# Optimization experiments

Hardware: AMD Instinct MI355X
Metric: run time of the kernel (lower is better)

## Reference

```python
import jax, jax.numpy as jnp
import numpy as np

B = 16384        # batch (population evaluation batch)
NUM_IN = 256     # input nodes
N = 1024         # total nodes
K = 8            # max fan-in (padded)
NN = N - NUM_IN  # non-input nodes, in topo order
NUM_OUT = 64


def setup_inputs() -> dict:
    key = jax.random.key(0)
    k0, k1, k2 = jax.random.split(key, 3)
    inputs = jax.random.normal(k0, (B, NUM_IN), dtype=jnp.float32)

    # Build a random DAG: node i (i >= NUM_IN) draws up to K predecessors from {0..i-1}.
    rng = np.random.default_rng(0)
    in_idx = np.zeros((NN, K), dtype=np.int32)
    edge_mask = np.zeros((NN, K), dtype=bool)
    for r in range(NN):
        node = NUM_IN + r
        deg = min(K, node)
        preds = rng.choice(node, size=deg, replace=False)
        in_idx[r, :deg] = preds
        edge_mask[r, :deg] = True

    edge_w = jax.random.normal(k1, (NN, K), dtype=jnp.float32) * 0.5
    bias = jax.random.normal(k2, (NN,), dtype=jnp.float32) * 0.1
    response = jnp.ones((NN,), dtype=jnp.float32)
    out_idx = jnp.arange(NUM_IN, N, dtype=jnp.int32)          # topo order of non-input nodes
    output_idx = jnp.arange(N - NUM_OUT, N, dtype=jnp.int32)  # output nodes
    return {
        "inputs": inputs, "edge_w": edge_w, "bias": bias, "response": response,
        "in_idx": jnp.asarray(in_idx), "edge_mask": jnp.asarray(edge_mask),
        "out_idx": out_idx, "output_idx": output_idx,
    }


def reference(inputs, edge_w, bias, response, in_idx, edge_mask, out_idx, output_idx):
    b = inputs.shape[0]
    num_in = inputs.shape[1]
    n = num_in + out_idx.shape[0]
    # node_vals[:, input_idx] = inputs  (input_idx == arange(num_in))
    node_vals = jnp.zeros((b, n), dtype=jnp.float32).at[:, :num_in].set(inputs)

    def step(carry, xs):
        idx_r, w_r, m_r, b_r, resp_r, o_r = xs
        # gather incoming node values [B, K], apply per-edge weight (conn gene)
        vals = carry[:, idx_r]
        s = jnp.sum(jnp.where(m_r, vals * w_r, 0.0), axis=1)  # node aggregation: sum
        y = jnp.tanh(b_r + resp_r * s)                        # node gene activation
        carry = carry.at[:, o_r].set(y)
        return carry, None

    node_vals, _ = jax.lax.scan(
        step, node_vals, (in_idx, edge_w, edge_mask, bias, response, out_idx)
    )
    return node_vals[:, output_idx]
```

## Files before the change

kernel.cpp:

```cpp
#include <hip/hip_runtime.h>
#include <stdint.h>
#include <stddef.h>

#define B_TOT   16384
#define NUM_IN  256
#define N_NODES 1024
#define NN      768
#define K       8
#define NUM_OUT 64
#define NB      64
#define MAXL    800
#define TPB     1024
#define WPB     16

typedef _Float16 h2 __attribute__((ext_vector_type(2)));

struct Rec {
  uint32_t p[8];
  uint32_t w01, w23, w45, w67;
  uint32_t outPh;
  float    bias;
  uint32_t pad0, pad1;
};
static_assert(sizeof(Rec) == 64, "Rec must be 64B");

__global__ __launch_bounds__(NN)
void setup_kernel(const int* __restrict__ in_idx,
                  const float* __restrict__ edge_w,
                  const float* __restrict__ bias,
                  const float* __restrict__ response,
                  const int* __restrict__ out_idx,
                  int* __restrict__ g_nlev,
                  int* __restrict__ g_loff,
                  Rec* __restrict__ recs)
{
  __shared__ int lvl[N_NODES];
  __shared__ int hist[MAXL];
  __shared__ int cnt[MAXL];
  __shared__ int offs[MAXL + 2];
  __shared__ int changed;
  __shared__ int maxlv;

  const int t = threadIdx.x;

  for (int i = t; i < N_NODES; i += NN) lvl[i] = 0;
  for (int i = t; i < MAXL; i += NN) { hist[i] = 0; cnt[i] = 0; }
  if (t == 0) maxlv = 0;

  int idxs[K];
#pragma unroll
  for (int k = 0; k < K; ++k)
    idxs[k] = in_idx[t * K + k];
  __syncthreads();

  for (int iter = 0; iter < 800; ++iter) {
    int nl = 0;
#pragma unroll
    for (int k = 0; k < K; ++k) {
      int l = lvl[idxs[k]];
      nl = (l > nl) ? l : nl;
    }
    nl += 1;
    __syncthreads();
    if (t == 0) changed = 0;
    int cur = lvl[NUM_IN + t];
    __syncthreads();
    if (nl != cur) { lvl[NUM_IN + t] = nl; changed = 1; }
    __syncthreads();
    if (changed == 0) break;
  }

  const int L = lvl[NUM_IN + t];
  atomicAdd(&hist[L], 1);
  atomicMax(&maxlv, L);
  __syncthreads();
  const int ml = maxlv;
  if (t == 0) {
    offs[1] = 0;
    for (int l = 1; l <= ml; ++l) offs[l + 1] = offs[l] + hist[l];
  }
  __syncthreads();
  const int pos = offs[L] + atomicAdd(&cnt[L], 1);

  Rec r;
#pragma unroll
  for (int k = 0; k < K; ++k) {
    uint32_t id = (uint32_t)idxs[k];
    r.p[k] = id * 64u + ((id & 31u) << 1);
  }
  const float rsp = response[t];
  uint16_t hw[K];
#pragma unroll
  for (int k = 0; k < K; ++k) {
    _Float16 h = (_Float16)(edge_w[t * K + k] * rsp);
    hw[k] = __builtin_bit_cast(uint16_t, h);
  }
  r.w01 = (uint32_t)hw[0] | ((uint32_t)hw[1] << 16);
  r.w23 = (uint32_t)hw[2] | ((uint32_t)hw[3] << 16);
  r.w45 = (uint32_t)hw[4] | ((uint32_t)hw[5] << 16);
  r.w67 = (uint32_t)hw[6] | ((uint32_t)hw[7] << 16);
  uint32_t oid = (uint32_t)out_idx[t];
  r.outPh = oid * 64u + ((oid & 31u) << 1);
  r.bias = bias[t];
  r.pad0 = 0; r.pad1 = 0;
  recs[pos] = r;

  if (t <= ml) g_loff[t] = offs[t + 1];
  if (t == 0)  g_nlev[0] = ml;
}

__global__ __launch_bounds__(TPB, 4)
void eval_kernel(const float* __restrict__ inputs,
                 const int* __restrict__ output_idx,
                 const int* __restrict__ g_nlev,
                 const int* __restrict__ g_loff,
                 const Rec* __restrict__ recs,
                 float* __restrict__ out)
{
  __shared__ _Float16 vals[N_NODES * NB];
  __shared__ int      loffs[MAXL + 1];

  const uint32_t tid  = threadIdx.x;
  const uint32_t lane = tid & 63u;
  const uint32_t wave = tid >> 6;
  const int      base = blockIdx.x * NB;

  const int nlev = g_nlev[0];
  for (int i = (int)tid; i <= nlev; i += TPB) loffs[i] = g_loff[i];

  const uint32_t col = tid & 255u;
  const uint32_t cg  = tid >> 8;
  const uint32_t swz = col * 64u + ((col & 31u) << 1);
  for (uint32_t c = cg; c < NB; c += 4) {
    float v = inputs[(size_t)(base + c) * NUM_IN + col];
    vals[swz ^ c] = (_Float16)v;
  }
  __syncthreads();

  for (int l = 0; l < nlev; ++l) {
    const int beg = loffs[l], end = loffs[l + 1];
    int j = beg + (int)wave;
    if (j < end) {
      Rec rr = recs[__builtin_amdgcn_readfirstlane(j)];
      for (;;) {
        const int jn = j + WPB;
        const bool has = jn < end;
        Rec rn;
        if (has) rn = recs[__builtin_amdgcn_readfirstlane(jn)];

        const _Float16 x0 = vals[rr.p[0] ^ lane];
        const _Float16 x1 = vals[rr.p[1] ^ lane];
        const _Float16 x2 = vals[rr.p[2] ^ lane];
        const _Float16 x3 = vals[rr.p[3] ^ lane];
        const _Float16 x4 = vals[rr.p[4] ^ lane];
        const _Float16 x5 = vals[rr.p[5] ^ lane];
        const _Float16 x6 = vals[rr.p[6] ^ lane];
        const _Float16 x7 = vals[rr.p[7] ^ lane];

        const h2 v01 = {x0, x1};
        const h2 v23 = {x2, x3};
        const h2 v45 = {x4, x5};
        const h2 v67 = {x6, x7};

#if __has_builtin(__builtin_amdgcn_fdot2)
        float x = rr.bias;
        x = __builtin_amdgcn_fdot2(v01, __builtin_bit_cast(h2, rr.w01), x, false);
        x = __builtin_amdgcn_fdot2(v23, __builtin_bit_cast(h2, rr.w23), x, false);
        x = __builtin_amdgcn_fdot2(v45, __builtin_bit_cast(h2, rr.w45), x, false);
        x = __builtin_amdgcn_fdot2(v67, __builtin_bit_cast(h2, rr.w67), x, false);
#else
        const h2 w01 = __builtin_bit_cast(h2, rr.w01);
        const h2 w23 = __builtin_bit_cast(h2, rr.w23);
        const h2 w45 = __builtin_bit_cast(h2, rr.w45);
        const h2 w67 = __builtin_bit_cast(h2, rr.w67);
        float s0 = __builtin_fmaf((float)w01.x, (float)v01.x, rr.bias);
        float s1 = (float)w01.y * (float)v01.y;
        float s2 = (float)w23.x * (float)v23.x;
        float s3 = (float)w23.y * (float)v23.y;
        s0 = __builtin_fmaf((float)w45.x, (float)v45.x, s0);
        s1 = __builtin_fmaf((float)w45.y, (float)v45.y, s1);
        s2 = __builtin_fmaf((float)w67.x, (float)v67.x, s2);
        s3 = __builtin_fmaf((float)w67.y, (float)v67.y, s3);
        float x = (s0 + s1) + (s2 + s3);
#endif

        const float e  = __expf(x + x);
        const float rc = __builtin_amdgcn_rcpf(e + 1.0f);
        const float y  = __builtin_fmaf(-2.0f, rc, 1.0f);

        vals[rr.outPh ^ lane] = (_Float16)y;

        if (!has) break;
        rr = rn; j = jn;
      }
    }
    __syncthreads();
  }

  const uint32_t oid  = (uint32_t)output_idx[lane];
  const uint32_t oswz = oid * 64u + ((oid & 31u) << 1);
  for (uint32_t k = 0; k < 4; ++k) {
    const uint32_t b = wave + k * 16u;
    float v = (float)vals[oswz ^ b];
    out[(size_t)(base + b) * NUM_OUT + lane] = v;
  }
}

extern "C" void kernel_launch(void* const* d_in, const int* in_sizes, int n_in,
                              void* d_out, int out_size, void* d_ws, size_t ws_size,
                              hipStream_t stream)
{
  (void)in_sizes; (void)n_in; (void)out_size; (void)ws_size;

  const float* inputs     = (const float*)d_in[0];
  const float* edge_w     = (const float*)d_in[1];
  const float* bias       = (const float*)d_in[2];
  const float* response   = (const float*)d_in[3];
  const int*   in_idx     = (const int*)d_in[4];
  const int*   out_idx    = (const int*)d_in[6];
  const int*   output_idx = (const int*)d_in[7];
  float*       out        = (float*)d_out;

  char* ws = (char*)d_ws;
  int* g_nlev = (int*)ws;
  int* g_loff = (int*)(ws + 256);
  Rec* recs   = (Rec*)(ws + 8192);

  hipLaunchKernelGGL(setup_kernel, dim3(1), dim3(NN), 0, stream,
                     in_idx, edge_w, bias, response, out_idx,
                     g_nlev, g_loff, recs);
  hipLaunchKernelGGL(eval_kernel, dim3(B_TOT / NB), dim3(TPB), 0, stream,
                     inputs, output_idx, g_nlev, g_loff, recs, out);
}
```

Before: 128.3 us.

## Software-pipeline LDS gathers across nodes, use byte offsets, double-buffer level setup

The eval loop now issues the next node's eight LDS gathers before computing the current node's dot product and tanh, so LDS latency overlaps with arithmetic. Precomputed offsets are stored as byte offsets to drop a shift per access. The setup kernel's level propagation moves to Jacobi-style double buffering and checks convergence only every fourth iteration, which cuts barriers. The risk is higher register pressure under the 4-waves launch bound. Within a level, loads of the next node are safe because nodes in the same level do not depend on each other.

```diff
diff --git a/kernel.cpp b/kernel.cpp
--- a/kernel.cpp
+++ b/kernel.cpp
@@ -34,7 +34,8 @@
                   int* __restrict__ g_loff,
                   Rec* __restrict__ recs)
 {
-  __shared__ int lvl[N_NODES];
+  __shared__ int lvlA[N_NODES];
+  __shared__ int lvlB[N_NODES];
   __shared__ int hist[MAXL];
   __shared__ int cnt[MAXL];
   __shared__ int offs[MAXL + 2];
@@ -43,7 +44,7 @@
 
   const int t = threadIdx.x;
 
-  for (int i = t; i < N_NODES; i += NN) lvl[i] = 0;
+  for (int i = t; i < N_NODES; i += NN) { lvlA[i] = 0; lvlB[i] = 0; }
   for (int i = t; i < MAXL; i += NN) { hist[i] = 0; cnt[i] = 0; }
   if (t == 0) maxlv = 0;
 
@@ -53,24 +54,32 @@
     idxs[k] = in_idx[t * K + k];
   __syncthreads();
 
-  for (int iter = 0; iter < 800; ++iter) {
+  int* cur = lvlA;
+  int* nxt = lvlB;
+  int L = 1;
+  for (int it = 0; it < 800; ++it) {
     int nl = 0;
 #pragma unroll
     for (int k = 0; k < K; ++k) {
-      int l = lvl[idxs[k]];
+      int l = cur[idxs[k]];
       nl = (l > nl) ? l : nl;
     }
     nl += 1;
-    __syncthreads();
-    if (t == 0) changed = 0;
-    int cur = lvl[NUM_IN + t];
-    __syncthreads();
-    if (nl != cur) { lvl[NUM_IN + t] = nl; changed = 1; }
-    __syncthreads();
-    if (changed == 0) break;
-  }
-
-  const int L = lvl[NUM_IN + t];
+    nxt[NUM_IN + t] = nl;
+    L = nl;
+    if ((it & 3) == 3) {
+      __syncthreads();
+      if (t == 0) changed = 0;
+      __syncthreads();
+      if (nl != cur[NUM_IN + t]) changed = 1;
+      __syncthreads();
+      if (changed == 0) break;
+    } else {
+      __syncthreads();
+    }
+    int* tmp = cur; cur = nxt; nxt = tmp;
+  }
+
   atomicAdd(&hist[L], 1);
   atomicMax(&maxlv, L);
   __syncthreads();
@@ -86,7 +95,7 @@
 #pragma unroll
   for (int k = 0; k < K; ++k) {
     uint32_t id = (uint32_t)idxs[k];
-    r.p[k] = id * 64u + ((id & 31u) << 1);
+    r.p[k] = (id * 64u + ((id & 31u) << 1)) << 1;
   }
   const float rsp = response[t];
   uint16_t hw[K];
@@ -100,7 +109,7 @@
   r.w45 = (uint32_t)hw[4] | ((uint32_t)hw[5] << 16);
   r.w67 = (uint32_t)hw[6] | ((uint32_t)hw[7] << 16);
   uint32_t oid = (uint32_t)out_idx[t];
-  r.outPh = oid * 64u + ((oid & 31u) << 1);
+  r.outPh = (oid * 64u + ((oid & 31u) << 1)) << 1;
   r.bias = bias[t];
   r.pad0 = 0; r.pad1 = 0;
   recs[pos] = r;
@@ -125,6 +134,10 @@
   const uint32_t wave = tid >> 6;
   const int      base = blockIdx.x * NB;
 
+  const char*  vbytes  = (const char*)vals;
+  char*        vbytesw = (char*)vals;
+  const uint32_t lane2 = lane << 1;
+
   const int nlev = g_nlev[0];
   for (int i = (int)tid; i <= nlev; i += TPB) loffs[i] = g_loff[i];
 
@@ -137,61 +150,71 @@
   }
   __syncthreads();
 
+#define LOADV(r, x0,x1,x2,x3,x4,x5,x6,x7) do {                      \
+    x0 = *(const _Float16*)(vbytes + ((r).p[0] ^ lane2));           \
+    x1 = *(const _Float16*)(vbytes + ((r).p[1] ^ lane2));           \
+    x2 = *(const _Float16*)(vbytes + ((r).p[2] ^ lane2));           \
+    x3 = *(const _Float16*)(vbytes + ((r).p[3] ^ lane2));           \
+    x4 = *(const _Float16*)(vbytes + ((r).p[4] ^ lane2));           \
+    x5 = *(const _Float16*)(vbytes + ((r).p[5] ^ lane2));           \
+    x6 = *(const _Float16*)(vbytes + ((r).p[6] ^ lane2));           \
+    x7 = *(const _Float16*)(vbytes + ((r).p[7] ^ lane2));           \
+  } while (0)
+
+#if __has_builtin(__builtin_amdgcn_fdot2)
+#define DOT8(r, x0,x1,x2,x3,x4,x5,x6,x7, xx) do {                                   \
+    h2 v01 = {x0, x1}, v23 = {x2, x3}, v45 = {x4, x5}, v67 = {x6, x7};              \
+    xx = (r).bias;                                                                  \
+    xx = __builtin_amdgcn_fdot2(v01, __builtin_bit_cast(h2, (r).w01), xx, false);   \
+    xx = __builtin_amdgcn_fdot2(v23, __builtin_bit_cast(h2, (r).w23), xx, false);   \
+    xx = __builtin_amdgcn_fdot2(v45, __builtin_bit_cast(h2, (r).w45), xx, false);   \
+    xx = __builtin_amdgcn_fdot2(v67, __builtin_bit_cast(h2, (r).w67), xx, false);   \
+  } while (0)
+#else
+#define DOT8(r, x0,x1,x2,x3,x4,x5,x6,x7, xx) do {                                   \
+    h2 w01 = __builtin_bit_cast(h2, (r).w01), w23 = __builtin_bit_cast(h2, (r).w23);\
+    h2 w45 = __builtin_bit_cast(h2, (r).w45), w67 = __builtin_bit_cast(h2, (r).w67);\
+    float s0 = __builtin_fmaf((float)w01.x, (float)x0, (r).bias);                   \
+    float s1 = (float)w01.y * (float)x1;                                            \
+    float s2 = (float)w23.x * (float)x2;                                            \
+    float s3 = (float)w23.y * (float)x3;                                            \
+    s0 = __builtin_fmaf((float)w45.x, (float)x4, s0);                               \
+    s1 = __builtin_fmaf((float)w45.y, (float)x5, s1);                               \
+    s2 = __builtin_fmaf((float)w67.x, (float)x6, s2);                               \
+    s3 = __builtin_fmaf((float)w67.y, (float)x7, s3);                               \
+    xx = (s0 + s1) + (s2 + s3);                                                     \
+  } while (0)
+#endif
+
+#define COMPUTE(r, x0,x1,x2,x3,x4,x5,x6,x7) do {                    \
+    float xx;                                                       \
+    DOT8(r, x0,x1,x2,x3,x4,x5,x6,x7, xx);                           \
+    const float e  = __expf(xx + xx);                               \
+    const float rc = __builtin_amdgcn_rcpf(e + 1.0f);               \
+    const float y  = __builtin_fmaf(-2.0f, rc, 1.0f);               \
+    *(_Float16*)(vbytesw + ((r).outPh ^ lane2)) = (_Float16)y;      \
+  } while (0)
+
   for (int l = 0; l < nlev; ++l) {
     const int beg = loffs[l], end = loffs[l + 1];
     int j = beg + (int)wave;
     if (j < end) {
-      Rec rr = recs[__builtin_amdgcn_readfirstlane(j)];
+      Rec rA = recs[__builtin_amdgcn_readfirstlane(j)];
+      _Float16 a0, a1, a2, a3, a4, a5, a6, a7;
+      LOADV(rA, a0, a1, a2, a3, a4, a5, a6, a7);
       for (;;) {
-        const int jn = j + WPB;
-        const bool has = jn < end;
-        Rec rn;
-        if (has) rn = recs[__builtin_amdgcn_readfirstlane(jn)];
-
-        const _Float16 x0 = vals[rr.p[0] ^ lane];
-        const _Float16 x1 = vals[rr.p[1] ^ lane];
-        const _Float16 x2 = vals[rr.p[2] ^ lane];
-        const _Float16 x3 = vals[rr.p[3] ^ lane];
-        const _Float16 x4 = vals[rr.p[4] ^ lane];
-        const _Float16 x5 = vals[rr.p[5] ^ lane];
-        const _Float16 x6 = vals[rr.p[6] ^ lane];
-        const _Float16 x7 = vals[rr.p[7] ^ lane];
-
-        const h2 v01 = {x0, x1};
-        const h2 v23 = {x2, x3};
-        const h2 v45 = {x4, x5};
-        const h2 v67 = {x6, x7};
-
-#if __has_builtin(__builtin_amdgcn_fdot2)
-        float x = rr.bias;
-        x = __builtin_amdgcn_fdot2(v01, __builtin_bit_cast(h2, rr.w01), x, false);
-        x = __builtin_amdgcn_fdot2(v23, __builtin_bit_cast(h2, rr.w23), x, false);
-        x = __builtin_amdgcn_fdot2(v45, __builtin_bit_cast(h2, rr.w45), x, false);
-        x = __builtin_amdgcn_fdot2(v67, __builtin_bit_cast(h2, rr.w67), x, false);
-#else
-        const h2 w01 = __builtin_bit_cast(h2, rr.w01);
-        const h2 w23 = __builtin_bit_cast(h2, rr.w23);
-        const h2 w45 = __builtin_bit_cast(h2, rr.w45);
-        const h2 w67 = __builtin_bit_cast(h2, rr.w67);
-        float s0 = __builtin_fmaf((float)w01.x, (float)v01.x, rr.bias);
-        float s1 = (float)w01.y * (float)v01.y;
-        float s2 = (float)w23.x * (float)v23.x;
-        float s3 = (float)w23.y * (float)v23.y;
-        s0 = __builtin_fmaf((float)w45.x, (float)v45.x, s0);
-        s1 = __builtin_fmaf((float)w45.y, (float)v45.y, s1);
-        s2 = __builtin_fmaf((float)w67.x, (float)v67.x, s2);
-        s3 = __builtin_fmaf((float)w67.y, (float)v67.y, s3);
-        float x = (s0 + s1) + (s2 + s3);
-#endif
-
-        const float e  = __expf(x + x);
-        const float rc = __builtin_amdgcn_rcpf(e + 1.0f);
-        const float y  = __builtin_fmaf(-2.0f, rc, 1.0f);
-
-        vals[rr.outPh ^ lane] = (_Float16)y;
-
-        if (!has) break;
-        rr = rn; j = jn;
+        int jn = j + WPB;
+        if (jn >= end) { COMPUTE(rA, a0, a1, a2, a3, a4, a5, a6, a7); break; }
+        Rec rB = recs[__builtin_amdgcn_readfirstlane(jn)];
+        _Float16 b0, b1, b2, b3, b4, b5, b6, b7;
+        LOADV(rB, b0, b1, b2, b3, b4, b5, b6, b7);
+        COMPUTE(rA, a0, a1, a2, a3, a4, a5, a6, a7);
+        j = jn; jn = j + WPB;
+        if (jn >= end) { COMPUTE(rB, b0, b1, b2, b3, b4, b5, b6, b7); break; }
+        rA = recs[__builtin_amdgcn_readfirstlane(jn)];
+        LOADV(rA, a0, a1, a2, a3, a4, a5, a6, a7);
+        COMPUTE(rB, b0, b1, b2, b3, b4, b5, b6, b7);
+        j = jn;
       }
     }
     __syncthreads();
```

Measured after the change: 126.1 us. No clear change (-1.7%).
